# Performance work log

Measured on AMD Instinct MI355X. Metric: run time of the kernel, lower is better.

## Reference

```python
import jax, jax.numpy as jnp
import numpy as np

SCALE = 100.0          # sigmoid sharpness used as soft comparator in long division
PRECISION_BITS = 16    # number of long-division iterations (ReciprocalFFN layers)


def setup_inputs() -> dict:
    key = jax.random.key(0)
    kq, kk, kv = jax.random.split(key, 3)
    B, D, N = 8192, 1024, 2048
    return {
        "query": jax.random.normal(kq, (B, D), dtype=jnp.float32),
        "keys": jax.random.normal(kk, (N, D), dtype=jnp.float32),
        "values": jax.random.normal(kv, (N, D), dtype=jnp.float32),
    }


def _reciprocal_scan(divisor):
    """16-step non-restoring long division computing ~1/divisor.

    Mirrors ReciprocalFFN: state = (remainder, quotient), remainder starts at 1,
    each step: doubled = 2*r; step = sigmoid(SCALE*(doubled - d));
    r' = doubled - d*step; q' = q + 2^{-(i+1)} * step.
    divisor: (B, 1) -> returns quotient (B, 1).
    """
    bit_weights = 2.0 ** -(jnp.arange(PRECISION_BITS, dtype=jnp.float32) + 1.0)

    def body(carry, w):
        r, q = carry
        doubled = r * 2.0
        step = jax.nn.sigmoid(SCALE * (doubled - divisor))
        return (doubled - divisor * step, q + w * step), None

    init = (jnp.ones_like(divisor), jnp.zeros_like(divisor))
    (_, quotient), _ = jax.lax.scan(body, init, bit_weights)
    return quotient


def reference(query, keys, values):
    # Baked-mode forward: QK scores -> softmax1 with FFN long-division reciprocal
    # -> weighted sum of values.
    scale = keys.shape[-1] ** -0.5
    scores = jnp.einsum("bd,nd->bn", query, keys) * scale          # (B, N)
    exps = jnp.exp(scores - jnp.max(scores, axis=-1, keepdims=True))
    sum_exp = 1.0 + jnp.sum(exps, axis=-1, keepdims=True)           # (B, 1)
    reciprocal = _reciprocal_scan(sum_exp)                          # (B, 1)
    weights = exps * reciprocal                                     # (B, N)
    return jnp.einsum("bn,nd->bd", weights, values)                 # (B, D)
```

## Files before the change

kernel.cpp:

```cpp
#include <hip/hip_runtime.h>
#include <hip/hip_bf16.h>
#include <stdint.h>
#include <math.h>

#define BQ   8192
#define DIM  1024
#define NK   2048

typedef unsigned short u16;
using f32x4  = __attribute__((ext_vector_type(4))) float;
using bf16x8 = __attribute__((ext_vector_type(8))) __bf16;
using f16x8  = __attribute__((ext_vector_type(8))) _Float16;
using u16x4  = __attribute__((ext_vector_type(4))) unsigned short;
using u16x8  = __attribute__((ext_vector_type(8))) unsigned short;

#define EXP_BIAS 4.0f


__device__ __forceinline__ u16 f2bf(float f) {
    uint32_t u = __float_as_uint(f);
    u += 0x7FFFu + ((u >> 16) & 1u);
    return (u16)(u >> 16);
}

__device__ __forceinline__ u16 f2h(float f) {
    _Float16 h = (_Float16)f;
    return __builtin_bit_cast(unsigned short, h);
}

__device__ __forceinline__ void gload_lds16(const void* g, void* l) {
    __builtin_amdgcn_global_load_lds(
        (const __attribute__((address_space(1))) void*)g,
        (__attribute__((address_space(3))) void*)l,
        16, 0, 0);
}

template<bool F16>
__device__ __forceinline__ f32x4 mfmaT(u16x8 a, u16x8 b, f32x4 c) {
    if constexpr (F16)
        return __builtin_amdgcn_mfma_f32_16x16x32_f16(
            __builtin_bit_cast(f16x8, a), __builtin_bit_cast(f16x8, b), c, 0, 0, 0);
    else
        return __builtin_amdgcn_mfma_f32_16x16x32_bf16(
            __builtin_bit_cast(bf16x8, a), __builtin_bit_cast(bf16x8, b), c, 0, 0, 0);
}


__global__ void cvt_qk(const float* __restrict__ Q, const float* __restrict__ K,
                       u16* __restrict__ Qb, u16* __restrict__ Kb, int n4Q, int n4T) {
    int i = blockIdx.x * blockDim.x + threadIdx.x;
    if (i >= n4T) return;
    const float* src; u16* dst; int j;
    if (i < n4Q) { src = Q; dst = Qb; j = i; }
    else         { src = K; dst = Kb; j = i - n4Q; }
    f32x4 v = reinterpret_cast<const f32x4*>(src)[j];
    u16x4 o;
    o.x = f2bf(v[0]); o.y = f2bf(v[1]); o.z = f2bf(v[2]); o.w = f2bf(v[3]);
    reinterpret_cast<u16x4*>(dst)[j] = o;
}

__global__ void transpose_cvt(const float* __restrict__ V, u16* __restrict__ VT) {
    __shared__ float tile[32][33];
    int d0 = blockIdx.x * 32;
    int n0 = blockIdx.y * 32;
    int tx = threadIdx.x, ty = threadIdx.y;
#pragma unroll
    for (int i = 0; i < 4; ++i)
        tile[ty + i * 8][tx] = V[(size_t)(n0 + ty + i * 8) * DIM + d0 + tx];
    __syncthreads();
#pragma unroll
    for (int i = 0; i < 4; ++i)
        VT[(size_t)(d0 + ty + i * 8) * NK + n0 + tx] = f2h(tile[tx][ty + i * 8]);
}


template<int BN, bool F16, bool EXPOUT, typename OT>
__global__ __launch_bounds__(512, 2)
void gemm256(const u16* __restrict__ A, const u16* __restrict__ B, OT* __restrict__ C,
             const float* __restrict__ rowFactor,
             int K, int lda, int ldb, int ldc, float scale, int nbn) {
    constexpr int WTN  = BN / 4;
    constexpr int NREP = BN / 64;
    constexpr int NH   = NREP / 2;
    constexpr int BCALLS = (BN == 256) ? 4 : 2;

    __shared__ u16 As[2][256 * 64];
    __shared__ u16 Bs[2][BN * 64];

    const int tid  = threadIdx.x;
    const int wave = tid >> 6;
    const int lane = tid & 63;
    const int wr = wave >> 2;
    const int wc = wave & 3;

    int id = blockIdx.x;
    const int cpx = gridDim.x >> 3;
    id = (id & 7) * cpx + (id >> 3);
    const int bm = id / nbn;
    const int bn = id % nbn;

    const int lsub  = lane >> 3;
    const int lslot = lane & 7;
    const int srcColEl = ((lslot ^ lsub) << 3);

    const int aRow0 = wr * 128 + wc * 32;
    int bRow0;
    if constexpr (BN == 256) bRow0 = (wc >> 1) * 128 + (wr * 2 + (wc & 1)) * 32;
    else                     bRow0 = wave * 16;

    const u16* aSrc = A + (size_t)(bm * 256 + aRow0 + lsub) * lda + srcColEl;
    const u16* bSrc = B + (size_t)(bn * BN  + bRow0 + lsub) * ldb + srcColEl;

    f32x4 acc[8][NREP] = {};

    const int NT = K >> 6;

    auto STAGE = [&](int buf, int kt) {
        const size_t ko = (size_t)kt * 64;
#pragma unroll
        for (int c2 = 0; c2 < 4; ++c2)
            gload_lds16(aSrc + (size_t)c2 * 8 * lda + ko, &As[buf][(aRow0 + c2 * 8) * 64]);
#pragma unroll
        for (int c2 = 0; c2 < BCALLS; ++c2)
            gload_lds16(bSrc + (size_t)c2 * 8 * ldb + ko, &Bs[buf][(bRow0 + c2 * 8) * 64]);
    };

    auto LDA_frag = [&](const char* base, int m, int kk) -> u16x8 {
        int r   = wr * 128 + m * 16 + (lane & 15);
        int off = r * 128 + (((kk * 64) + ((lane >> 4) << 4)) ^ ((lane & 7) << 4));
        return *reinterpret_cast<const u16x8*>(base + off);
    };
    auto LDB_frag = [&](const char* base, int n, int kk) -> u16x8 {
        int r   = wc * WTN + n * 16 + (lane & 15);
        int off = r * 128 + (((kk * 64) + ((lane >> 4) << 4)) ^ ((lane & 7) << 4));
        return *reinterpret_cast<const u16x8*>(base + off);
    };

    STAGE(0, 0);
    __syncthreads();

    int cbuf = 0;
    for (int t = 0; t < NT; ++t) {
        if (t + 1 < NT) STAGE(cbuf ^ 1, t + 1);
        __builtin_amdgcn_sched_barrier(0);

        const char* aB = (const char*)&As[cbuf][0];
        const char* bB = (const char*)&Bs[cbuf][0];

        u16x8 af[4][2];
        u16x8 bf0[NH][2], bf1[NH][2];

#pragma unroll
        for (int mi = 0; mi < 4; ++mi) { af[mi][0] = LDA_frag(aB, mi, 0); af[mi][1] = LDA_frag(aB, mi, 1); }
#pragma unroll
        for (int ni = 0; ni < NH; ++ni) { bf0[ni][0] = LDB_frag(bB, ni, 0); bf0[ni][1] = LDB_frag(bB, ni, 1); }
        __builtin_amdgcn_s_setprio(1);
#pragma unroll
        for (int mi = 0; mi < 4; ++mi)
#pragma unroll
            for (int ni = 0; ni < NH; ++ni) {
                acc[mi][ni] = mfmaT<F16>(af[mi][0], bf0[ni][0], acc[mi][ni]);
                acc[mi][ni] = mfmaT<F16>(af[mi][1], bf0[ni][1], acc[mi][ni]);
            }
        __builtin_amdgcn_s_setprio(0);

#pragma unroll
        for (int ni = 0; ni < NH; ++ni) { bf1[ni][0] = LDB_frag(bB, NH + ni, 0); bf1[ni][1] = LDB_frag(bB, NH + ni, 1); }
        __builtin_amdgcn_s_setprio(1);
#pragma unroll
        for (int mi = 0; mi < 4; ++mi)
#pragma unroll
            for (int ni = 0; ni < NH; ++ni) {
                acc[mi][NH + ni] = mfmaT<F16>(af[mi][0], bf1[ni][0], acc[mi][NH + ni]);
                acc[mi][NH + ni] = mfmaT<F16>(af[mi][1], bf1[ni][1], acc[mi][NH + ni]);
            }
        __builtin_amdgcn_s_setprio(0);

#pragma unroll
        for (int mi = 0; mi < 4; ++mi) { af[mi][0] = LDA_frag(aB, 4 + mi, 0); af[mi][1] = LDA_frag(aB, 4 + mi, 1); }
        __builtin_amdgcn_s_setprio(1);
#pragma unroll
        for (int mi = 0; mi < 4; ++mi)
#pragma unroll
            for (int ni = 0; ni < NH; ++ni) {
                acc[4 + mi][NH + ni] = mfmaT<F16>(af[mi][0], bf1[ni][0], acc[4 + mi][NH + ni]);
                acc[4 + mi][NH + ni] = mfmaT<F16>(af[mi][1], bf1[ni][1], acc[4 + mi][NH + ni]);
            }
        __builtin_amdgcn_s_setprio(0);

        __builtin_amdgcn_s_setprio(1);
#pragma unroll
        for (int mi = 0; mi < 4; ++mi)
#pragma unroll
            for (int ni = 0; ni < NH; ++ni) {
                acc[4 + mi][ni] = mfmaT<F16>(af[mi][0], bf0[ni][0], acc[4 + mi][ni]);
                acc[4 + mi][ni] = mfmaT<F16>(af[mi][1], bf0[ni][1], acc[4 + mi][ni]);
            }
        __builtin_amdgcn_s_setprio(0);

        __syncthreads();
        cbuf ^= 1;
    }

    const int col0 = bn * BN + wc * WTN + (lane & 15);
    const int row0 = bm * 256 + wr * 128 + ((lane >> 4) << 2);
#pragma unroll
    for (int m = 0; m < 8; ++m) {
#pragma unroll
        for (int j = 0; j < 4; ++j) {
            int row = row0 + m * 16 + j;
            float rf = (rowFactor != nullptr) ? rowFactor[row] : 1.0f;
            OT* cp = C + (size_t)row * ldc + col0;
#pragma unroll
            for (int n = 0; n < NREP; ++n) {
                float v = acc[m][n][j] * scale;
                if constexpr (EXPOUT) v = expf(v - EXP_BIAS);
                cp[n * 16] = (OT)(v * rf);
            }
        }
    }
}


__global__ __launch_bounds__(256)
void row_stats(const u16* __restrict__ E, float* __restrict__ factor) {
    const int lane = threadIdx.x & 63;
    const int row  = blockIdx.x * 4 + (threadIdx.x >> 6);

    const u16x8* sp = reinterpret_cast<const u16x8*>(E + (size_t)row * NK);
    u16x8 raw[4];
#pragma unroll
    for (int j = 0; j < 4; ++j) raw[j] = sp[lane + j * 64];

    float T = 0.f, mx = 0.f;
#pragma unroll
    for (int j = 0; j < 4; ++j)
#pragma unroll
        for (int i = 0; i < 8; ++i) {
            float f = (float)__builtin_bit_cast(_Float16, (unsigned short)raw[j][i]);
            T += f;
            mx = fmaxf(mx, f);
        }
#pragma unroll
    for (int off = 32; off; off >>= 1) {
        T  += __shfl_xor(T, off);
        mx  = fmaxf(mx, __shfl_xor(mx, off));
    }

    const float d = 1.0f + T / mx;

    float r = 1.0f, q = 0.0f, w = 0.5f;
#pragma unroll
    for (int i = 0; i < 16; ++i) {
        float doubled = 2.0f * r;
        float st = 1.0f / (1.0f + expf(-100.0f * (doubled - d)));
        r = doubled - d * st;
        q += w * st;
        w *= 0.5f;
    }

    if (lane == 0) factor[row] = q / mx;
}


extern "C" void kernel_launch(void* const* d_in, const int* in_sizes, int n_in,
                              void* d_out, int out_size, void* d_ws, size_t ws_size,
                              hipStream_t stream) {
    const float* Q = (const float*)d_in[0];
    const float* K = (const float*)d_in[1];
    const float* V = (const float*)d_in[2];
    float* out = (float*)d_out;

    char* ws = (char*)d_ws;
    u16*   Qb     = (u16*)(ws);
    u16*   Kb     = (u16*)(ws + (16u << 20));
    u16*   VhT    = (u16*)(ws + (20u << 20));
    u16*   E      = (u16*)(ws + (24u << 20));
    float* factor = (float*)(ws + (56u << 20));

    {
        int n4Q = BQ * DIM / 4;
        int n4T = n4Q + NK * DIM / 4;
        cvt_qk<<<(n4T + 255) / 256, 256, 0, stream>>>(Q, K, Qb, Kb, n4Q, n4T);
    }
    transpose_cvt<<<dim3(DIM / 32, NK / 32), dim3(32, 8), 0, stream>>>(V, VhT);

    gemm256<256, false, true, _Float16><<<(BQ / 256) * (NK / 256), 512, 0, stream>>>(
        Qb, Kb, (_Float16*)E, nullptr, DIM, DIM, DIM, NK, 0.03125f, NK / 256);

    row_stats<<<BQ / 4, 256, 0, stream>>>(E, factor);

    gemm256<128, true, false, float><<<(BQ / 256) * (DIM / 128), 512, 0, stream>>>(
        E, VhT, out, factor, NK, NK, NK, DIM, 1.0f, DIM / 128);
}
```

Baseline: 108.3 us.

## Fuse row sum/max statistics into first GEMM epilogue, drop separate stats pass

```diff
diff --git a/kernel.cpp b/kernel.cpp
--- a/kernel.cpp
+++ b/kernel.cpp
@@ -74,10 +74,11 @@
 }
 
 
-template<int BN, bool F16, bool EXPOUT, typename OT>
+template<int BN, bool F16, bool EXPOUT, bool STATS, bool HASF, typename OT>
 __global__ __launch_bounds__(512, 2)
 void gemm256(const u16* __restrict__ A, const u16* __restrict__ B, OT* __restrict__ C,
              const float* __restrict__ rowFactor,
+             float* __restrict__ pSum, float* __restrict__ pMax,
              int K, int lda, int ldb, int ldc, float scale, int nbn) {
     constexpr int WTN  = BN / 4;
     constexpr int NREP = BN / 64;
@@ -154,7 +155,6 @@
         for (int mi = 0; mi < 4; ++mi) { af[mi][0] = LDA_frag(aB, mi, 0); af[mi][1] = LDA_frag(aB, mi, 1); }
 #pragma unroll
         for (int ni = 0; ni < NH; ++ni) { bf0[ni][0] = LDB_frag(bB, ni, 0); bf0[ni][1] = LDB_frag(bB, ni, 1); }
-        __builtin_amdgcn_s_setprio(1);
 #pragma unroll
         for (int mi = 0; mi < 4; ++mi)
 #pragma unroll
@@ -162,11 +162,9 @@
                 acc[mi][ni] = mfmaT<F16>(af[mi][0], bf0[ni][0], acc[mi][ni]);
                 acc[mi][ni] = mfmaT<F16>(af[mi][1], bf0[ni][1], acc[mi][ni]);
             }
-        __builtin_amdgcn_s_setprio(0);
 
 #pragma unroll
         for (int ni = 0; ni < NH; ++ni) { bf1[ni][0] = LDB_frag(bB, NH + ni, 0); bf1[ni][1] = LDB_frag(bB, NH + ni, 1); }
-        __builtin_amdgcn_s_setprio(1);
 #pragma unroll
         for (int mi = 0; mi < 4; ++mi)
 #pragma unroll
@@ -174,11 +172,9 @@
                 acc[mi][NH + ni] = mfmaT<F16>(af[mi][0], bf1[ni][0], acc[mi][NH + ni]);
                 acc[mi][NH + ni] = mfmaT<F16>(af[mi][1], bf1[ni][1], acc[mi][NH + ni]);
             }
-        __builtin_amdgcn_s_setprio(0);
 
 #pragma unroll
         for (int mi = 0; mi < 4; ++mi) { af[mi][0] = LDA_frag(aB, 4 + mi, 0); af[mi][1] = LDA_frag(aB, 4 + mi, 1); }
-        __builtin_amdgcn_s_setprio(1);
 #pragma unroll
         for (int mi = 0; mi < 4; ++mi)
 #pragma unroll
@@ -186,9 +182,7 @@
                 acc[4 + mi][NH + ni] = mfmaT<F16>(af[mi][0], bf1[ni][0], acc[4 + mi][NH + ni]);
                 acc[4 + mi][NH + ni] = mfmaT<F16>(af[mi][1], bf1[ni][1], acc[4 + mi][NH + ni]);
             }
-        __builtin_amdgcn_s_setprio(0);
-
-        __builtin_amdgcn_s_setprio(1);
+
 #pragma unroll
         for (int mi = 0; mi < 4; ++mi)
 #pragma unroll
@@ -196,7 +190,6 @@
                 acc[4 + mi][ni] = mfmaT<F16>(af[mi][0], bf0[ni][0], acc[4 + mi][ni]);
                 acc[4 + mi][ni] = mfmaT<F16>(af[mi][1], bf0[ni][1], acc[4 + mi][ni]);
             }
-        __builtin_amdgcn_s_setprio(0);
 
         __syncthreads();
         cbuf ^= 1;
@@ -208,43 +201,44 @@
     for (int m = 0; m < 8; ++m) {
 #pragma unroll
         for (int j = 0; j < 4; ++j) {
-            int row = row0 + m * 16 + j;
-            float rf = (rowFactor != nullptr) ? rowFactor[row] : 1.0f;
+            const int row = row0 + m * 16 + j;
+            float rf = 1.0f;
+            if constexpr (HASF) rf = rowFactor[row];
             OT* cp = C + (size_t)row * ldc + col0;
+            float psum = 0.f, pmx = 0.f;
 #pragma unroll
             for (int n = 0; n < NREP; ++n) {
                 float v = acc[m][n][j] * scale;
                 if constexpr (EXPOUT) v = expf(v - EXP_BIAS);
+                if constexpr (STATS) { psum += v; pmx = fmaxf(pmx, v); }
                 cp[n * 16] = (OT)(v * rf);
             }
+            if constexpr (STATS) {
+#pragma unroll
+                for (int off = 1; off < 16; off <<= 1) {
+                    psum += __shfl_xor(psum, off);
+                    pmx   = fmaxf(pmx, __shfl_xor(pmx, off));
+                }
+                if ((lane & 15) == 0) {
+                    const int slot = bn * 4 + wc;
+                    pSum[(size_t)slot * BQ + row] = psum;
+                    pMax[(size_t)slot * BQ + row] = pmx;
+                }
+            }
         }
     }
 }
 
 
 __global__ __launch_bounds__(256)
-void row_stats(const u16* __restrict__ E, float* __restrict__ factor) {
-    const int lane = threadIdx.x & 63;
-    const int row  = blockIdx.x * 4 + (threadIdx.x >> 6);
-
-    const u16x8* sp = reinterpret_cast<const u16x8*>(E + (size_t)row * NK);
-    u16x8 raw[4];
-#pragma unroll
-    for (int j = 0; j < 4; ++j) raw[j] = sp[lane + j * 64];
-
+void finalize_factor(const float* __restrict__ pSum, const float* __restrict__ pMax,
+                     float* __restrict__ factor) {
+    const int row = blockIdx.x * 256 + threadIdx.x;
     float T = 0.f, mx = 0.f;
 #pragma unroll
-    for (int j = 0; j < 4; ++j)
-#pragma unroll
-        for (int i = 0; i < 8; ++i) {
-            float f = (float)__builtin_bit_cast(_Float16, (unsigned short)raw[j][i]);
-            T += f;
-            mx = fmaxf(mx, f);
-        }
-#pragma unroll
-    for (int off = 32; off; off >>= 1) {
-        T  += __shfl_xor(T, off);
-        mx  = fmaxf(mx, __shfl_xor(mx, off));
+    for (int s = 0; s < 32; ++s) {
+        T  += pSum[(size_t)s * BQ + row];
+        mx  = fmaxf(mx, pMax[(size_t)s * BQ + row]);
     }
 
     const float d = 1.0f + T / mx;
@@ -259,7 +253,7 @@
         w *= 0.5f;
     }
 
-    if (lane == 0) factor[row] = q / mx;
+    factor[row] = q / mx;
 }
 
 
@@ -276,7 +270,9 @@
     u16*   Kb     = (u16*)(ws + (16u << 20));
     u16*   VhT    = (u16*)(ws + (20u << 20));
     u16*   E      = (u16*)(ws + (24u << 20));
-    float* factor = (float*)(ws + (56u << 20));
+    float* pSum   = (float*)(ws + (56u << 20));
+    float* pMax   = (float*)(ws + (57u << 20));
+    float* factor = (float*)(ws + (58u << 20));
 
     {
         int n4Q = BQ * DIM / 4;
@@ -285,11 +281,13 @@
     }
     transpose_cvt<<<dim3(DIM / 32, NK / 32), dim3(32, 8), 0, stream>>>(V, VhT);
 
-    gemm256<256, false, true, _Float16><<<(BQ / 256) * (NK / 256), 512, 0, stream>>>(
-        Qb, Kb, (_Float16*)E, nullptr, DIM, DIM, DIM, NK, 0.03125f, NK / 256);
-
-    row_stats<<<BQ / 4, 256, 0, stream>>>(E, factor);
-
-    gemm256<128, true, false, float><<<(BQ / 256) * (DIM / 128), 512, 0, stream>>>(
-        E, VhT, out, factor, NK, NK, NK, DIM, 1.0f, DIM / 128);
-}
+    gemm256<256, false, true, true, false, _Float16>
+        <<<(BQ / 256) * (NK / 256), 512, 0, stream>>>(
+        Qb, Kb, (_Float16*)E, nullptr, pSum, pMax, DIM, DIM, DIM, NK, 0.03125f, NK / 256);
+
+    finalize_factor<<<BQ / 256, 256, 0, stream>>>(pSum, pMax, factor);
+
+    gemm256<128, true, false, false, true, float>
+        <<<(BQ / 256) * (DIM / 128), 512, 0, stream>>>(
+        E, VhT, out, factor, nullptr, nullptr, NK, NK, NK, DIM, 1.0f, DIM / 128);
+}
```

New measurement: 112.9 us. +4.3%, slower.
